# Performance work log

Hardware: AMD Instinct MI355X
Metric: run time of the kernel (lower is better)

## Reference

```python
import jax, jax.numpy as jnp
import numpy as np

B, N, A = 8, 16384, 7
NUM_GROUP = 1024   # npoint / G
GROUP_SIZE = 32    # knn k / M


def setup_inputs() -> dict:
    key = jax.random.key(0)
    xyz = jax.random.uniform(key, (B, N, A), dtype=jnp.float32)
    return {"xyz": xyz}


def _farthest_point_sample(xyz, npoint):
    # xyz: [B, N, A]; distances computed on first 3 dims only.
    b, n, a = xyz.shape
    coords = xyz[:, :, :3]
    batch = jnp.arange(b)
    # Deterministic start index (original uses randint; any start is a valid FPS seed).
    init = (jnp.full((b, n), 1e10, dtype=xyz.dtype), jnp.zeros((b,), dtype=jnp.int32))

    def step(carry, _):
        distance, farthest = carry
        centroid = xyz[batch, farthest]                      # [B, A]
        d = jnp.sum((coords - centroid[:, None, :3]) ** 2, -1)  # [B, N]
        distance = jnp.minimum(distance, d)                  # masked update == min
        new_farthest = jnp.argmax(distance, axis=-1).astype(jnp.int32)
        return (distance, new_farthest), (farthest, centroid)

    _, (idxs, cents) = jax.lax.scan(step, init, None, length=npoint)
    centroids = jnp.swapaxes(idxs, 0, 1)        # [B, npoint]
    centroids_attrs = jnp.swapaxes(cents, 0, 1)  # [B, npoint, A]
    return centroids, centroids_attrs


def _knn(center, xyz, k):
    # Euclidean cdist over ALL A attributes (as in the original torch.cdist call).
    # Squared distance preserves topk ordering.
    c2 = jnp.sum(center ** 2, -1)[:, :, None]    # [B, G, 1]
    x2 = jnp.sum(xyz ** 2, -1)[:, None, :]       # [B, 1, N]
    d2 = c2 + x2 - 2.0 * jnp.einsum('bga,bna->bgn', center, xyz)  # [B, G, N]
    _, idx = jax.lax.top_k(-d2, k)               # smallest-k, ascending distance
    return idx


def reference(xyz):
    center_idx, centroids_attrs = _farthest_point_sample(xyz, NUM_GROUP)
    centroids_coors = centroids_attrs[:, :, :3]
    idx = _knn(centroids_attrs, xyz, GROUP_SIZE)             # [B, G, M]
    b = xyz.shape[0]
    neighborhood = xyz[jnp.arange(b)[:, None, None], idx]    # [B, G, M, A]
    neighborhood = jnp.concatenate(
        [neighborhood[..., :3] - centroids_coors[:, :, None, :],
         neighborhood[..., 3:]], axis=-1)
    return neighborhood, center_idx, centroids_attrs, centroids_coors
```

## Files before the change

kernel.cpp:

```cpp
#include <hip/hip_runtime.h>

#define N_PTS  16384
#define B_SZ   8
#define NGROUP 1024
#define KNN_K  32
#define ATTR   7

#define OFF_NB     0
#define OFF_IDX    (B_SZ * NGROUP * KNN_K * ATTR)
#define OFF_CATTR  (OFF_IDX + B_SZ * NGROUP)
#define OFF_CCOORD (OFF_CATTR + B_SZ * NGROUP * ATTR)

typedef float f2u __attribute__((ext_vector_type(2), aligned(4)));

__global__ void prep_kernel(const float* __restrict__ xyz, float* __restrict__ x2,
                            float* __restrict__ xt) {
#pragma clang fp contract(off)
    int i = blockIdx.x * blockDim.x + threadIdx.x;
    if (i >= B_SZ * N_PTS) return;
    const int b = i >> 14;
    const int p = i & (N_PTS - 1);
    const float* q = xyz + (size_t)i * ATTR;
    f2u a01 = *(const f2u*)q;
    f2u a23 = *(const f2u*)(q + 2);
    f2u a45 = *(const f2u*)(q + 4);
    float a6 = q[6];
    float s = a01.x * a01.x;
    s = s + a01.y * a01.y;
    s = s + a23.x * a23.x;
    s = s + a23.y * a23.y;
    s = s + a45.x * a45.x;
    s = s + a45.y * a45.y;
    s = s + a6 * a6;
    x2[i] = s;
    float* T = xt + (size_t)b * ATTR * N_PTS + p;
    T[0 * N_PTS] = a01.x;
    T[1 * N_PTS] = a01.y;
    T[2 * N_PTS] = a23.x;
    T[3 * N_PTS] = a23.y;
    T[4 * N_PTS] = a45.x;
    T[5 * N_PTS] = a45.y;
    T[6 * N_PTS] = a6;
}

__global__ __launch_bounds__(1024) __attribute__((amdgpu_waves_per_eu(4, 4)))
void fps_kernel(const float* __restrict__ xyz, float* __restrict__ out) {
#pragma clang fp contract(off)
    const int b = blockIdx.x;
    const int t = threadIdx.x;
    const int lane = t & 63;
    const float* X = xyz + (size_t)b * N_PTS * ATTR;

    float px[16], py[16], pz[16], pd[16];
#pragma unroll
    for (int j = 0; j < 16; ++j) {
        const int p = t + (j << 10);
        const float* q = X + (size_t)p * ATTR;
        f2u u = *(const f2u*)q;
        px[j] = u.x; py[j] = u.y; pz[j] = q[2];
        pd[j] = 1e10f;
    }

    __shared__ unsigned long long slot[3];
    __shared__ int sel[NGROUP];
    if (t == 0) { slot[0] = 0ull; sel[0] = 0; }
    float cx = X[0], cy = X[1], cz = X[2];
    __syncthreads();

    for (int s = 0; s < NGROUP - 1; ++s) {
        float m0 = -1.0f, m1 = -1.0f;
#pragma unroll
        for (int j = 0; j < 16; j += 2) {
            {
                float dx = px[j] - cx;
                float dy = py[j] - cy;
                float dz = pz[j] - cz;
                float a  = dx * dx + dy * dy;
                a = a + dz * dz;
                float nd = fminf(pd[j], a);
                pd[j] = nd;
                m0 = fmaxf(m0, nd);
            }
            {
                float dx = px[j + 1] - cx;
                float dy = py[j + 1] - cy;
                float dz = pz[j + 1] - cz;
                float a  = dx * dx + dy * dy;
                a = a + dz * dz;
                float nd = fminf(pd[j + 1], a);
                pd[j + 1] = nd;
                m1 = fmaxf(m1, nd);
            }
        }
        const float tmax = fmaxf(m0, m1);
        float wmax = tmax;
#pragma unroll
        for (int off = 1; off < 64; off <<= 1)
            wmax = fmaxf(wmax, __shfl_xor(wmax, off));
        int myp = 0x7fffffff;
        if (tmax == wmax) {
#pragma unroll
            for (int j = 15; j >= 0; --j)
                if (pd[j] == wmax) myp = t + (j << 10);
        }
        unsigned long long m = __ballot(tmax == wmax);
        int wp = __shfl(myp, __ffsll(m) - 1);
        if (__popcll(m) > 1) {
            unsigned long long mm = m;
            while (mm) {
                int l = __ffsll(mm) - 1; mm &= mm - 1;
                int pp = __shfl(myp, l);
                wp = min(wp, pp);
            }
        }
        if (lane == 0)
            atomicMax(&slot[s % 3],
                      ((unsigned long long)__float_as_uint(wmax) << 32) |
                      (unsigned)(N_PTS - wp));
        if (t == 0) slot[(s + 1) % 3] = 0ull;
        __syncthreads();
        const unsigned long long key = slot[s % 3];
        int bidx = N_PTS - (int)(unsigned)key;
        bidx = __builtin_amdgcn_readfirstlane(bidx);
        if (t == 0) sel[s + 1] = bidx;
        const float* q = X + (size_t)bidx * ATTR;
        cx = q[0]; cy = q[1]; cz = q[2];
    }
    __syncthreads();

    {
        const int g = t;
        const int idx = sel[g];
        const float* q = X + (size_t)idx * ATTR;
        float a0 = q[0], a1 = q[1], a2 = q[2], a3 = q[3], a4 = q[4], a5 = q[5], a6 = q[6];
        out[OFF_IDX + b * NGROUP + g] = (float)idx;
        float* ca = out + OFF_CATTR + (size_t)(b * NGROUP + g) * ATTR;
        ca[0] = a0; ca[1] = a1; ca[2] = a2; ca[3] = a3; ca[4] = a4; ca[5] = a5; ca[6] = a6;
        float* cc = out + OFF_CCOORD + (size_t)(b * NGROUP + g) * 3;
        cc[0] = a0; cc[1] = a1; cc[2] = a2;
    }
}

__device__ __forceinline__ void topk_insert(float d2, int p, int lane,
                                            float& ld, int& li, float& kd, int& ki) {
    const bool cand = (d2 < kd) || (d2 == kd && p < ki);
    unsigned long long mask = __ballot(cand);
    while (mask) {
        const int l = __ffsll(mask) - 1;
        mask &= mask - 1;
        const float dc = __shfl(d2, l);
        const int   pc = __shfl(p, l);
        if ((dc < kd) || (dc == kd && pc < ki)) {
            const bool before = (ld < dc) || (ld == dc && li < pc);
            const int pos = (int)__popcll(__ballot(before));
            const float sd = __shfl_up(ld, 1);
            const int   si = __shfl_up(li, 1);
            if (lane == pos)      { ld = dc; li = pc; }
            else if (lane > pos)  { ld = sd; li = si; }
            if (lane >= KNN_K)    { ld = __builtin_inff(); li = 0x7fffffff; }
            kd = __shfl(ld, KNN_K - 1);
            ki = __shfl(li, KNN_K - 1);
        }
    }
}

__global__ __launch_bounds__(512) void knn_lds_kernel(const float* __restrict__ xyz,
                                                      const float* __restrict__ x2,
                                                      const float* __restrict__ xt,
                                                      float* __restrict__ out) {
#pragma clang fp contract(off)
    const int lane = threadIdx.x & 63;
    const int w = threadIdx.x >> 6;
    const int g0 = blockIdx.x * 16 + w;
    const int b  = (blockIdx.x * 16) >> 10;
    const float* X = xyz + (size_t)b * N_PTS * ATTR;

    __shared__ float Ts[8][1024];

    float c[2][7], csq[2], ld[2], kd[2];
    int li[2], ki[2];
#pragma unroll
    for (int g = 0; g < 2; ++g) {
        const int gg = g0 + g * 8;
        const float* C = out + OFF_CATTR + (size_t)gg * ATTR;
#pragma unroll
        for (int a = 0; a < ATTR; ++a) c[g][a] = C[a];
        float s = c[g][0] * c[g][0];
        s = s + c[g][1] * c[g][1];
        s = s + c[g][2] * c[g][2];
        s = s + c[g][3] * c[g][3];
        s = s + c[g][4] * c[g][4];
        s = s + c[g][5] * c[g][5];
        s = s + c[g][6] * c[g][6];
        csq[g] = s;
        ld[g] = __builtin_inff(); li[g] = 0x7fffffff;
        kd[g] = __builtin_inff(); ki[g] = 0x7fffffff;
    }

    for (int tile = 0; tile < N_PTS / 1024; ++tile) {
        {
            const float* src = (w < ATTR)
                ? (xt + ((size_t)b * ATTR + w) * N_PTS + tile * 1024)
                : (x2 + (size_t)b * N_PTS + tile * 1024);
            const float4* s4 = (const float4*)src;
            float4* dst = (float4*)Ts[w];
#pragma unroll
            for (int j = 0; j < 4; ++j) dst[j * 64 + lane] = s4[j * 64 + lane];
        }
        __syncthreads();

        for (int it = 0; it < 4; ++it) {
            const int lbase = it * 256 + lane * 4;
            const int pbase = tile * 1024 + lbase;
            float vq[8][4];
#pragma unroll
            for (int a = 0; a < 8; ++a) {
                float4 tv = *(const float4*)&Ts[a][lbase];
                vq[a][0] = tv.x; vq[a][1] = tv.y; vq[a][2] = tv.z; vq[a][3] = tv.w;
            }
#pragma unroll
            for (int g = 0; g < 2; ++g) {
                float d2r[4];
                bool anyc = false;
#pragma unroll
                for (int r = 0; r < 4; ++r) {
                    float dot = c[g][0] * vq[0][r];
                    dot = dot + c[g][1] * vq[1][r];
                    dot = dot + c[g][2] * vq[2][r];
                    dot = dot + c[g][3] * vq[3][r];
                    dot = dot + c[g][4] * vq[4][r];
                    dot = dot + c[g][5] * vq[5][r];
                    dot = dot + c[g][6] * vq[6][r];
                    d2r[r] = (csq[g] + vq[7][r]) - 2.0f * dot;
                    const int p = pbase + r;
                    anyc = anyc || (d2r[r] < kd[g]) || (d2r[r] == kd[g] && p < ki[g]);
                }
                if (__ballot(anyc)) {
#pragma unroll
                    for (int r = 0; r < 4; ++r)
                        topk_insert(d2r[r], pbase + r, lane, ld[g], li[g], kd[g], ki[g]);
                }
            }
        }
        __syncthreads();
    }

#pragma unroll
    for (int g = 0; g < 2; ++g) {
        if (lane < KNN_K) {
            const int gg = g0 + g * 8;
            const float* q = X + (size_t)li[g] * ATTR;
            float* o = out + OFF_NB + ((size_t)gg * KNN_K + lane) * ATTR;
            o[0] = q[0] - c[g][0];
            o[1] = q[1] - c[g][1];
            o[2] = q[2] - c[g][2];
            o[3] = q[3];
            o[4] = q[4];
            o[5] = q[5];
            o[6] = q[6];
        }
    }
}

__global__ __launch_bounds__(256) void knn_fallback(const float* __restrict__ xyz,
                                                    float* __restrict__ out) {
#pragma clang fp contract(off)
    const int lane = threadIdx.x & 63;
    const int gg = blockIdx.x * 4 + (threadIdx.x >> 6);
    const int b  = gg >> 10;
    const float* X = xyz + (size_t)b * N_PTS * ATTR;
    const float* C = out + OFF_CATTR + (size_t)gg * ATTR;
    const float c0 = C[0], c1 = C[1], c2a = C[2], c3 = C[3], c4 = C[4], c5 = C[5], c6 = C[6];
    float csq = c0 * c0;
    csq = csq + c1 * c1;
    csq = csq + c2a * c2a;
    csq = csq + c3 * c3;
    csq = csq + c4 * c4;
    csq = csq + c5 * c5;
    csq = csq + c6 * c6;
    float ld = __builtin_inff(); int li = 0x7fffffff;
    float kd = __builtin_inff(); int ki = 0x7fffffff;
    for (int p0 = 0; p0 < N_PTS; p0 += 64) {
        const int p = p0 + lane;
        const float* q = X + (size_t)p * ATTR;
        float dot = c0 * q[0];
        dot = dot + c1 * q[1];
        dot = dot + c2a * q[2];
        dot = dot + c3 * q[3];
        dot = dot + c4 * q[4];
        dot = dot + c5 * q[5];
        dot = dot + c6 * q[6];
        float xx = q[0] * q[0];
        xx = xx + q[1] * q[1];
        xx = xx + q[2] * q[2];
        xx = xx + q[3] * q[3];
        xx = xx + q[4] * q[4];
        xx = xx + q[5] * q[5];
        xx = xx + q[6] * q[6];
        const float d2 = (csq + xx) - 2.0f * dot;
        topk_insert(d2, p, lane, ld, li, kd, ki);
    }
    if (lane < KNN_K) {
        const float* q = X + (size_t)li * ATTR;
        float* o = out + OFF_NB + ((size_t)gg * KNN_K + lane) * ATTR;
        o[0] = q[0] - c0;
        o[1] = q[1] - c1;
        o[2] = q[2] - c2a;
        o[3] = q[3];
        o[4] = q[4];
        o[5] = q[5];
        o[6] = q[6];
    }
}

extern "C" void kernel_launch(void* const* d_in, const int* in_sizes, int n_in,
                              void* d_out, int out_size, void* d_ws, size_t ws_size,
                              hipStream_t stream) {
    const float* xyz = (const float*)d_in[0];
    float* out = (float*)d_out;

    const size_t need = (size_t)(B_SZ * N_PTS) * (1 + ATTR) * sizeof(float);
    const bool use_ws = ws_size >= need;
    float* x2 = use_ws ? (float*)d_ws : nullptr;
    float* xt = use_ws ? ((float*)d_ws + B_SZ * N_PTS) : nullptr;

    if (use_ws) {
        prep_kernel<<<(B_SZ * N_PTS + 255) / 256, 256, 0, stream>>>(xyz, x2, xt);
    }
    fps_kernel<<<B_SZ, 1024, 0, stream>>>(xyz, out);
    if (use_ws) {
        knn_lds_kernel<<<(B_SZ * NGROUP) / 16, 512, 0, stream>>>(xyz, x2, xt, out);
    } else {
        knn_fallback<<<(B_SZ * NGROUP) / 4, 256, 0, stream>>>(xyz, out);
    }
}
```

Baseline: 2.299 ms.

## Halve FPS block size and replace LDS atomicMax with per-wave slots plus shuffle reduce

The FPS kernel now runs 512 threads per batch instead of 1024, with each thread holding 32 points in registers. The per-step block-wide argmax no longer uses an LDS 64-bit atomicMax into a rotating 3-slot buffer. Each wave writes its packed key into a double-buffered per-wave slot, and after the barrier every wave reduces the 8 keys with xor shuffles. The goal is to cut barrier and atomic contention in the serial 1023-step loop, at the cost of more register pressure and more serial distance work per thread.

```diff
diff --git a/kernel.cpp b/kernel.cpp
--- a/kernel.cpp
+++ b/kernel.cpp
@@ -43,56 +43,68 @@
     T[6 * N_PTS] = a6;
 }
 
-__global__ __launch_bounds__(1024) __attribute__((amdgpu_waves_per_eu(4, 4)))
+__global__ __launch_bounds__(512) __attribute__((amdgpu_waves_per_eu(2, 2)))
 void fps_kernel(const float* __restrict__ xyz, float* __restrict__ out) {
 #pragma clang fp contract(off)
     const int b = blockIdx.x;
     const int t = threadIdx.x;
     const int lane = t & 63;
+    const int w = t >> 6;
     const float* X = xyz + (size_t)b * N_PTS * ATTR;
 
-    float px[16], py[16], pz[16], pd[16];
-#pragma unroll
-    for (int j = 0; j < 16; ++j) {
-        const int p = t + (j << 10);
+    float px[32], py[32], pz[32], pd[32];
+#pragma unroll
+    for (int j = 0; j < 32; ++j) {
+        const int p = t + (j << 9);
         const float* q = X + (size_t)p * ATTR;
         f2u u = *(const f2u*)q;
         px[j] = u.x; py[j] = u.y; pz[j] = q[2];
         pd[j] = 1e10f;
     }
 
-    __shared__ unsigned long long slot[3];
+    __shared__ unsigned long long slot2[2][8];
     __shared__ int sel[NGROUP];
-    if (t == 0) { slot[0] = 0ull; sel[0] = 0; }
+    if (t == 0) sel[0] = 0;
     float cx = X[0], cy = X[1], cz = X[2];
-    __syncthreads();
 
     for (int s = 0; s < NGROUP - 1; ++s) {
-        float m0 = -1.0f, m1 = -1.0f;
-#pragma unroll
-        for (int j = 0; j < 16; j += 2) {
+        float m0 = -1.0f, m1 = -1.0f, m2 = -1.0f, m3 = -1.0f;
+#pragma unroll
+        for (int j = 0; j < 32; j += 4) {
             {
-                float dx = px[j] - cx;
-                float dy = py[j] - cy;
-                float dz = pz[j] - cz;
-                float a  = dx * dx + dy * dy;
+                float dx = px[j] - cx, dy = py[j] - cy, dz = pz[j] - cz;
+                float a = dx * dx + dy * dy;
                 a = a + dz * dz;
                 float nd = fminf(pd[j], a);
                 pd[j] = nd;
                 m0 = fmaxf(m0, nd);
             }
             {
-                float dx = px[j + 1] - cx;
-                float dy = py[j + 1] - cy;
-                float dz = pz[j + 1] - cz;
-                float a  = dx * dx + dy * dy;
+                float dx = px[j + 1] - cx, dy = py[j + 1] - cy, dz = pz[j + 1] - cz;
+                float a = dx * dx + dy * dy;
                 a = a + dz * dz;
                 float nd = fminf(pd[j + 1], a);
                 pd[j + 1] = nd;
                 m1 = fmaxf(m1, nd);
             }
-        }
-        const float tmax = fmaxf(m0, m1);
+            {
+                float dx = px[j + 2] - cx, dy = py[j + 2] - cy, dz = pz[j + 2] - cz;
+                float a = dx * dx + dy * dy;
+                a = a + dz * dz;
+                float nd = fminf(pd[j + 2], a);
+                pd[j + 2] = nd;
+                m2 = fmaxf(m2, nd);
+            }
+            {
+                float dx = px[j + 3] - cx, dy = py[j + 3] - cy, dz = pz[j + 3] - cz;
+                float a = dx * dx + dy * dy;
+                a = a + dz * dz;
+                float nd = fminf(pd[j + 3], a);
+                pd[j + 3] = nd;
+                m3 = fmaxf(m3, nd);
+            }
+        }
+        const float tmax = fmaxf(fmaxf(m0, m1), fmaxf(m2, m3));
         float wmax = tmax;
 #pragma unroll
         for (int off = 1; off < 64; off <<= 1)
@@ -100,8 +112,8 @@
         int myp = 0x7fffffff;
         if (tmax == wmax) {
 #pragma unroll
-            for (int j = 15; j >= 0; --j)
-                if (pd[j] == wmax) myp = t + (j << 10);
+            for (int j = 31; j >= 0; --j)
+                if (pd[j] == wmax) myp = t + (j << 9);
         }
         unsigned long long m = __ballot(tmax == wmax);
         int wp = __shfl(myp, __ffsll(m) - 1);
@@ -114,12 +126,16 @@
             }
         }
         if (lane == 0)
-            atomicMax(&slot[s % 3],
-                      ((unsigned long long)__float_as_uint(wmax) << 32) |
-                      (unsigned)(N_PTS - wp));
-        if (t == 0) slot[(s + 1) % 3] = 0ull;
+            slot2[s & 1][w] =
+                ((unsigned long long)__float_as_uint(wmax) << 32) |
+                (unsigned)(N_PTS - wp);
         __syncthreads();
-        const unsigned long long key = slot[s % 3];
+        unsigned long long key = slot2[s & 1][lane & 7];
+#pragma unroll
+        for (int off = 1; off < 8; off <<= 1) {
+            unsigned long long ok = __shfl_xor(key, off);
+            if (ok > key) key = ok;
+        }
         int bidx = N_PTS - (int)(unsigned)key;
         bidx = __builtin_amdgcn_readfirstlane(bidx);
         if (t == 0) sel[s + 1] = bidx;
@@ -128,8 +144,7 @@
     }
     __syncthreads();
 
-    {
-        const int g = t;
+    for (int g = t; g < NGROUP; g += 512) {
         const int idx = sel[g];
         const float* q = X + (size_t)idx * ATTR;
         float a0 = q[0], a1 = q[1], a2 = q[2], a3 = q[3], a4 = q[4], a5 = q[5], a6 = q[6];
@@ -327,7 +342,7 @@
     if (use_ws) {
         prep_kernel<<<(B_SZ * N_PTS + 255) / 256, 256, 0, stream>>>(xyz, x2, xt);
     }
-    fps_kernel<<<B_SZ, 1024, 0, stream>>>(xyz, out);
+    fps_kernel<<<B_SZ, 512, 0, stream>>>(xyz, out);
     if (use_ws) {
         knn_lds_kernel<<<(B_SZ * NGROUP) / 16, 512, 0, stream>>>(xyz, x2, xt, out);
     } else {
```

Result: slower. 2.461 ms (+7.0%).
